# Kernel tuning notes

Measured on AMD Instinct MI355X. Metric: run time of the kernel, lower is better.

The kernel has to match this reference:

```python
import jax, jax.numpy as jnp
import numpy as np

N = 100000
E = 1600000
IN_FEATS = 256
OUT_FEATS = 128
THRESHOLD = 0.5


def setup_inputs() -> dict:
    key = jax.random.key(0)
    k1, k2, k3, k4, k5, k6, k7 = jax.random.split(key, 7)
    return {
        "feat": jax.random.normal(k1, (N, IN_FEATS), dtype=jnp.float32),
        "src": jax.random.randint(k2, (E,), 0, N, dtype=jnp.int32),
        "dst": jax.random.randint(k3, (E,), 0, N, dtype=jnp.int32),
        "edge_weight": jax.random.uniform(k4, (E,), dtype=jnp.float32),
        "weight": jax.random.normal(k5, (IN_FEATS, OUT_FEATS), dtype=jnp.float32),
        "bias": jax.random.normal(k6, (OUT_FEATS,), dtype=jnp.float32),
        "mask_real": jax.random.uniform(k7, (IN_FEATS, OUT_FEATS), dtype=jnp.float32),
    }


def reference(feat, src, dst, edge_weight, weight, bias, mask_real):
    ones_e = jnp.ones((E,), dtype=feat.dtype)
    # norm == 'both': scale source feats by out_degree^-0.5 (clamped at 1)
    out_deg = jnp.clip(jax.ops.segment_sum(ones_e, src, num_segments=N), 1.0)
    feat_src = feat * (out_deg ** -0.5)[:, None]  # [N, IN]
    # binarized mask with straight-through estimator (training-mode path)
    hard = (mask_real > THRESHOLD).astype(mask_real.dtype)
    mask_t = jax.lax.stop_gradient(hard - mask_real) + mask_real
    w = mask_t * weight  # [IN, OUT]
    # in_feats > out_feats: project before aggregation
    feat_src = feat_src @ w  # [N, OUT]
    # u_mul_e then sum: gather source feats, scale by edge weight, scatter-add to dst
    msgs = feat_src[src] * edge_weight[:, None]  # [E, OUT]
    rst = jax.ops.segment_sum(msgs, dst, num_segments=N)  # [N, OUT]
    # norm == 'both': scale by in_degree^-0.5 (clamped at 1)
    in_deg = jnp.clip(jax.ops.segment_sum(ones_e, dst, num_segments=N), 1.0)
    rst = rst * (in_deg ** -0.5)[:, None]
    return rst + bias
```

## Files before the change

### kernel.cpp

```cpp
#include <hip/hip_runtime.h>

#define N_NODES 100000
#define N_EDGES 1600000
#define IN_F 256
#define OUT_F 128
#define NBUCK 391
#define NPART 256
#define CHUNK (N_EDGES / NPART)
#define BCAP 5632

#define ODW2 12500
#define ODRB2 ((ODW2 + 255) / 256)

typedef __attribute__((ext_vector_type(8))) short short8;
typedef __attribute__((ext_vector_type(4))) float f32x4;

__device__ __forceinline__ unsigned bf16_rne(float f) {
    unsigned u = __float_as_uint(f);
    return (u + 0x7fffu + ((u >> 16) & 1u)) >> 16;
}

__global__ __launch_bounds__(1024) void fused_pre_kernel(const int* __restrict__ src,
                                                         const int* __restrict__ dst,
                                                         const float* __restrict__ weight,
                                                         const float* __restrict__ mask_real,
                                                         unsigned* __restrict__ part,
                                                         unsigned* __restrict__ hist,
                                                         unsigned short* __restrict__ wmT) {
    __shared__ unsigned h[ODW2];
    __shared__ unsigned hh[NBUCK];
    int b = blockIdx.x, t = threadIdx.x;
    for (int i = t; i < ODW2; i += 1024) h[i] = 0u;
    for (int i = t; i < NBUCK; i += 1024) hh[i] = 0u;
    if (t < 128) {
        int i = b * 128 + t;
        int k = i >> 7, n = i & 127;
        float v = (mask_real[i] > 0.5f) ? weight[i] : 0.0f;
        wmT[(size_t)n * IN_F + k] = (unsigned short)bf16_rne(v);
    }
    __syncthreads();
    int base = b * CHUNK;
    for (int i = t; i < CHUNK; i += 1024) {
        unsigned s = (unsigned)src[base + i];
        unsigned d = (unsigned)dst[base + i];
        atomicAdd(&h[s >> 3], 1u << ((s & 7u) * 4u));
        atomicAdd(&hh[d >> 8], 1u);
    }
    __syncthreads();
    unsigned* op = part + (size_t)b * ODW2;
    for (int i = t; i < ODW2; i += 1024) op[i] = h[i];
    for (int i = t; i < NBUCK; i += 1024) hist[(size_t)b * NBUCK + i] = hh[i];
}

__global__ __launch_bounds__(256) void fused_reduce_kernel(const unsigned* __restrict__ part,
                                                           const unsigned* __restrict__ hist,
                                                           unsigned* __restrict__ outpk,
                                                           unsigned* __restrict__ bsum,
                                                           unsigned* __restrict__ colscan) {
    __shared__ unsigned pscan[256];
    int t = threadIdx.x;
    if (blockIdx.x < ODRB2) {
        int d = blockIdx.x * 256 + t;
        if (d < ODW2) {
            unsigned sumE = 0u, sumO = 0u;
#pragma unroll 8
            for (int p = 0; p < NPART; p++) {
                unsigned v = part[(size_t)p * ODW2 + d];
                sumE += v & 0x0F0F0F0Fu;
                sumO += (v >> 4) & 0x0F0F0F0Fu;
            }
            unsigned w0 = (sumE & 0xFFu) | ((sumO & 0xFFu) << 8) |
                          ((sumE & 0xFF00u) << 8) | ((sumO & 0xFF00u) << 16);
            unsigned w1 = ((sumE >> 16) & 0xFFu) | (((sumO >> 16) & 0xFFu) << 8) |
                          (((sumE >> 24) & 0xFFu) << 16) | ((sumO >> 24) << 24);
            ((uint2*)outpk)[d] = make_uint2(w0, w1);
        }
    } else {
        int b = blockIdx.x - ODRB2;
        unsigned v = hist[(size_t)t * NBUCK + b];
        pscan[t] = v;
        __syncthreads();
#pragma unroll
        for (int d = 1; d < 256; d <<= 1) {
            unsigned x = (t >= d) ? pscan[t - d] : 0u;
            __syncthreads();
            pscan[t] += x;
            __syncthreads();
        }
        colscan[(size_t)b * 256 + t] = pscan[t] - v;
        if (t == 255) bsum[b] = pscan[255];
    }
}

__global__ __launch_bounds__(1024) void scatter_kernel(const int* __restrict__ src,
                                                       const int* __restrict__ dst,
                                                       const float* __restrict__ ew,
                                                       const unsigned* __restrict__ colscan,
                                                       const unsigned* __restrict__ bsum,
                                                       uint2* __restrict__ tmp) {
    __shared__ unsigned sc[1024];
    __shared__ unsigned cur[NBUCK];
    int p = blockIdx.x, t = threadIdx.x;
    unsigned v = (t < NBUCK) ? bsum[t] : 0u;
    sc[t] = v;
    __syncthreads();
#pragma unroll
    for (int d = 1; d < 1024; d <<= 1) {
        unsigned x = (t >= d) ? sc[t - d] : 0u;
        __syncthreads();
        sc[t] += x;
        __syncthreads();
    }
    if (t < NBUCK) cur[t] = (sc[t] - v) + colscan[(size_t)t * 256 + p];
    __syncthreads();
    int base = p * CHUNK;
    for (int i = t; i < CHUNK; i += 1024) {
        int e = base + i;
        int s = src[e];
        int d = dst[e];
        unsigned pos = atomicAdd(&cur[(unsigned)d >> 8], 1u);
        tmp[pos] = make_uint2((unsigned)s | (((unsigned)d & 255u) << 17),
                              __float_as_uint(ew[e]));
    }
}

__global__ __launch_bounds__(512) void gemm_kernel(const float* __restrict__ feat,
                                                   const unsigned short* __restrict__ wmT,
                                                   const unsigned char* __restrict__ outdeg8,
                                                   unsigned short* __restrict__ hb) {
    __shared__ unsigned short sB[128][264];
    int t = threadIdx.x;
    for (int idx = t; idx < (128 * 256 / 8); idx += 512) {
        int flat = idx * 8;
        *(uint4*)&sB[flat >> 8][flat & 255] = *(const uint4*)&wmT[flat];
    }
    __syncthreads();

    int lane = t & 63, wv = t >> 6;
    int m16 = lane & 15, quad = lane >> 4;
    int row0 = blockIdx.x * 128;
    int arow = min(row0 + wv * 16 + m16, N_NODES - 1);
    const float* fp = feat + (size_t)arow * IN_F + quad * 8;

    float4 va[16];
#pragma unroll
    for (int i = 0; i < 8; i++) {
        va[2 * i]     = *(const float4*)(fp + i * 32);
        va[2 * i + 1] = *(const float4*)(fp + i * 32 + 4);
    }

    f32x4 acc[8];
#pragma unroll
    for (int i = 0; i < 8; i++) acc[i] = (f32x4){0.f, 0.f, 0.f, 0.f};

#pragma unroll
    for (int i = 0; i < 8; i++) {
        uint4 pk;
        pk.x = bf16_rne(va[2 * i].x) | (bf16_rne(va[2 * i].y) << 16);
        pk.y = bf16_rne(va[2 * i].z) | (bf16_rne(va[2 * i].w) << 16);
        pk.z = bf16_rne(va[2 * i + 1].x) | (bf16_rne(va[2 * i + 1].y) << 16);
        pk.w = bf16_rne(va[2 * i + 1].z) | (bf16_rne(va[2 * i + 1].w) << 16);
        short8 a;
        *(uint4*)&a = pk;
#pragma unroll
        for (int nt = 0; nt < 8; nt++) {
            short8 b = *(const short8*)&sB[nt * 16 + m16][i * 32 + quad * 8];
            acc[nt] = __builtin_amdgcn_mfma_f32_16x16x32_bf16(a, b, acc[nt], 0, 0, 0);
        }
    }
#pragma unroll
    for (int reg = 0; reg < 4; reg++) {
        int row = row0 + wv * 16 + quad * 4 + reg;
        if (row < N_NODES) {
            float s = rsqrtf(fmaxf((float)outdeg8[row], 1.0f));
#pragma unroll
            for (int nt = 0; nt < 8; nt++)
                hb[(size_t)row * OUT_F + nt * 16 + m16] =
                    (unsigned short)bf16_rne(acc[nt][reg] * s);
        }
    }
}

__global__ __launch_bounds__(1024) void bucket_gather_kernel(const uint2* __restrict__ tmp,
                                                             const unsigned* __restrict__ bsum,
                                                             const uint4* __restrict__ hrows4,
                                                             const float* __restrict__ bias,
                                                             float* __restrict__ out) {
    __shared__ uint2 ebuf[BCAP];
    __shared__ unsigned sm[BCAP];
    __shared__ unsigned nstart[257];
    __shared__ unsigned hcnt[256];
    __shared__ unsigned red[1024];
    int b = blockIdx.x, t = threadIdx.x;

    unsigned loc = 0u;
    for (int i = t; i < b; i += 1024) loc += bsum[i];
    red[t] = loc;
    __syncthreads();
#pragma unroll
    for (int d = 512; d > 0; d >>= 1) {
        if (t < d) red[t] += red[t + d];
        __syncthreads();
    }
    unsigned base = red[0];
    unsigned next = base + bsum[b];
    int cnt = (int)(next - base);
    if (cnt > BCAP) cnt = BCAP;
    if (t < 256) hcnt[t] = 0u;
    for (int i = t; i < cnt; i += 1024) ebuf[i] = tmp[base + i];
    __syncthreads();
    for (int i = t; i < cnt; i += 1024) atomicAdd(&hcnt[ebuf[i].x >> 17], 1u);
    __syncthreads();
    unsigned v = (t < 256) ? hcnt[t] : 0u;
    if (t < 256) red[t] = v;
    __syncthreads();
#pragma unroll
    for (int d = 1; d < 256; d <<= 1) {
        unsigned x = (t < 256 && t >= d) ? red[t - d] : 0u;
        __syncthreads();
        if (t < 256) red[t] += x;
        __syncthreads();
    }
    if (t < 256) {
        unsigned excl = red[t] - v;
        nstart[t] = excl;
        hcnt[t] = excl;
    }
    if (t == 0) nstart[256] = (unsigned)cnt;
    __syncthreads();
    for (int i = t; i < cnt; i += 1024) {
        uint2 m = ebuf[i];
        unsigned pos = atomicAdd(&hcnt[m.x >> 17], 1u);
        sm[pos] = ((m.y + 0x10000u) & 0xFFFE0000u) | (m.x & 0x1FFFFu);
    }
    __syncthreads();

    int lane = t & 63, wv = t >> 6;
    int g = lane >> 4, q = lane & 15;
    for (int nn = wv * 16; nn < wv * 16 + 16; nn++) {
        int node = b * 256 + nn;
        if (node >= N_NODES) continue;
        unsigned beg = nstart[nn];
        int deg = (int)(nstart[nn + 1] - beg);

        float acc[8];
#pragma unroll
        for (int i = 0; i < 8; i++) acc[i] = 0.0f;

        for (int bs = 0; bs < deg; bs += 64) {
            int c = min(64, deg - bs);
            unsigned pv = (lane < c) ? sm[beg + bs + lane] : 0u;
            int nch = (c + 3) >> 2;
#pragma unroll 4
            for (int j = 0; j < nch; j++) {
                int ei = (j << 2) + g;
                unsigned p = __shfl(pv, ei);
                unsigned s = p & 0x1FFFFu;
                float w = __uint_as_float(p & 0xFFFE0000u);
                uint4 h = hrows4[(size_t)s * 16u + q];
                acc[0] = fmaf(__uint_as_float(h.x << 16), w, acc[0]);
                acc[1] = fmaf(__uint_as_float(h.x & 0xffff0000u), w, acc[1]);
                acc[2] = fmaf(__uint_as_float(h.y << 16), w, acc[2]);
                acc[3] = fmaf(__uint_as_float(h.y & 0xffff0000u), w, acc[3]);
                acc[4] = fmaf(__uint_as_float(h.z << 16), w, acc[4]);
                acc[5] = fmaf(__uint_as_float(h.z & 0xffff0000u), w, acc[5]);
                acc[6] = fmaf(__uint_as_float(h.w << 16), w, acc[6]);
                acc[7] = fmaf(__uint_as_float(h.w & 0xffff0000u), w, acc[7]);
            }
        }

#pragma unroll
        for (int i = 0; i < 8; i++) {
            acc[i] += __shfl_xor(acc[i], 16);
            acc[i] += __shfl_xor(acc[i], 32);
        }

        float o0, o1;
        if (g == 0)      { o0 = acc[0]; o1 = acc[1]; }
        else if (g == 1) { o0 = acc[2]; o1 = acc[3]; }
        else if (g == 2) { o0 = acc[4]; o1 = acc[5]; }
        else             { o0 = acc[6]; o1 = acc[7]; }

        float scale = rsqrtf(fmaxf((float)deg, 1.0f));
        int col = q * 8 + g * 2;
        float2 bb = *(const float2*)&bias[col];
        float2 o = make_float2(o0 * scale + bb.x, o1 * scale + bb.y);
        *(float2*)&out[(size_t)node * OUT_F + col] = o;
    }
}

extern "C" void kernel_launch(void* const* d_in, const int* in_sizes, int n_in,
                              void* d_out, int out_size, void* d_ws, size_t ws_size,
                              hipStream_t stream) {
    const float* feat      = (const float*)d_in[0];
    const int*   src       = (const int*)d_in[1];
    const int*   dst       = (const int*)d_in[2];
    const float* ew        = (const float*)d_in[3];
    const float* weight    = (const float*)d_in[4];
    const float* bias      = (const float*)d_in[5];
    const float* mask_real = (const float*)d_in[6];
    float* out = (float*)d_out;

    char* ws = (char*)d_ws;
    size_t o = 0;
    auto take = [&](size_t bytes) {
        char* p = ws + o;
        o = (o + bytes + 255) & ~(size_t)255;
        return p;
    };
    unsigned short* wmT     = (unsigned short*)take((size_t)IN_F * OUT_F * 2);
    unsigned*       outpk   = (unsigned*)take((size_t)25600 * 4);
    unsigned*       hist    = (unsigned*)take((size_t)NPART * NBUCK * 4);
    unsigned*       colscan = (unsigned*)take((size_t)NBUCK * 256 * 4);
    unsigned*       bsum    = (unsigned*)take((size_t)NBUCK * 4);
    uint2*          tmp     = (uint2*)take((size_t)N_EDGES * 8);
    unsigned short* hrows   = (unsigned short*)take((size_t)N_NODES * OUT_F * 2);

    unsigned* odpart = (unsigned*)tmp;

    fused_pre_kernel<<<NPART, 1024, 0, stream>>>(src, dst, weight, mask_real,
                                                 odpart, hist, wmT);
    fused_reduce_kernel<<<ODRB2 + NBUCK, 256, 0, stream>>>(odpart, hist, outpk,
                                                           bsum, colscan);
    scatter_kernel<<<NPART, 1024, 0, stream>>>(src, dst, ew, colscan, bsum, tmp);
    gemm_kernel<<<(N_NODES + 127) / 128, 512, 0, stream>>>(feat, wmT,
                                                           (const unsigned char*)outpk, hrows);
    bucket_gather_kernel<<<NBUCK, 1024, 0, stream>>>(tmp, bsum,
                                                     (const uint4*)hrows, bias, out);
}
```

Baseline: 300.6 us.

## Fuse degree, scan and scatter phases into one cooperative kernel; drop GEMM LDS staging

The pre-histogram, reduce/scan and edge scatter kernels are merged into a single cooperative kernel that uses grid-wide syncs between phases. This removes two kernel launches and the idle gaps between them. Separately, the GEMM no longer stages the masked weight matrix in LDS. It reads B fragments straight from global/L2 memory with smaller 256-thread blocks, and a sched_barrier keeps the feature loads grouped. The costs are the grid-sync overhead, a need for all 256 large blocks to be co-resident, and more global-memory traffic for B in the GEMM.

```diff
diff --git a/kernel.cpp b/kernel.cpp
--- a/kernel.cpp
+++ b/kernel.cpp
@@ -1,4 +1,7 @@
 #include <hip/hip_runtime.h>
+#include <hip/hip_cooperative_groups.h>
+
+namespace cg = cooperative_groups;
 
 #define N_NODES 100000
 #define N_EDGES 1600000
@@ -10,7 +13,6 @@
 #define BCAP 5632
 
 #define ODW2 12500
-#define ODRB2 ((ODW2 + 255) / 256)
 
 typedef __attribute__((ext_vector_type(8))) short short8;
 typedef __attribute__((ext_vector_type(4))) float f32x4;
@@ -20,16 +22,24 @@
     return (u + 0x7fffu + ((u >> 16) & 1u)) >> 16;
 }
 
-__global__ __launch_bounds__(1024) void fused_pre_kernel(const int* __restrict__ src,
-                                                         const int* __restrict__ dst,
-                                                         const float* __restrict__ weight,
-                                                         const float* __restrict__ mask_real,
-                                                         unsigned* __restrict__ part,
-                                                         unsigned* __restrict__ hist,
-                                                         unsigned short* __restrict__ wmT) {
+__global__ __launch_bounds__(1024) void prep_kernel(const int* __restrict__ src,
+                                                    const int* __restrict__ dst,
+                                                    const float* __restrict__ ew,
+                                                    const float* __restrict__ weight,
+                                                    const float* __restrict__ mask_real,
+                                                    unsigned* __restrict__ odpart,
+                                                    unsigned* __restrict__ hist,
+                                                    unsigned short* __restrict__ wmT,
+                                                    unsigned* __restrict__ outpk,
+                                                    unsigned* __restrict__ bsum,
+                                                    unsigned* __restrict__ colscan,
+                                                    uint2* __restrict__ tmp) {
+    cg::grid_group grid = cg::this_grid();
     __shared__ unsigned h[ODW2];
     __shared__ unsigned hh[NBUCK];
+    __shared__ unsigned sc[1024];
     int b = blockIdx.x, t = threadIdx.x;
+
     for (int i = t; i < ODW2; i += 1024) h[i] = 0u;
     for (int i = t; i < NBUCK; i += 1024) hh[i] = 0u;
     if (t < 128) {
@@ -47,25 +57,21 @@
         atomicAdd(&hh[d >> 8], 1u);
     }
     __syncthreads();
-    unsigned* op = part + (size_t)b * ODW2;
-    for (int i = t; i < ODW2; i += 1024) op[i] = h[i];
-    for (int i = t; i < NBUCK; i += 1024) hist[(size_t)b * NBUCK + i] = hh[i];
-}
-
-__global__ __launch_bounds__(256) void fused_reduce_kernel(const unsigned* __restrict__ part,
-                                                           const unsigned* __restrict__ hist,
-                                                           unsigned* __restrict__ outpk,
-                                                           unsigned* __restrict__ bsum,
-                                                           unsigned* __restrict__ colscan) {
-    __shared__ unsigned pscan[256];
-    int t = threadIdx.x;
-    if (blockIdx.x < ODRB2) {
-        int d = blockIdx.x * 256 + t;
-        if (d < ODW2) {
+    {
+        unsigned* op = odpart + (size_t)b * ODW2;
+        for (int i = t; i < ODW2; i += 1024) op[i] = h[i];
+        for (int i = t; i < NBUCK; i += 1024) hist[(size_t)b * NBUCK + i] = hh[i];
+    }
+
+    grid.sync();
+
+    if (b < 25) {
+        int d = b * 512 + t;
+        if (t < 512 && d < ODW2) {
             unsigned sumE = 0u, sumO = 0u;
 #pragma unroll 8
             for (int p = 0; p < NPART; p++) {
-                unsigned v = part[(size_t)p * ODW2 + d];
+                unsigned v = odpart[(size_t)p * ODW2 + d];
                 sumE += v & 0x0F0F0F0Fu;
                 sumO += (v >> 4) & 0x0F0F0F0Fu;
             }
@@ -76,71 +82,60 @@
             ((uint2*)outpk)[d] = make_uint2(w0, w1);
         }
     } else {
-        int b = blockIdx.x - ODRB2;
-        unsigned v = hist[(size_t)t * NBUCK + b];
-        pscan[t] = v;
-        __syncthreads();
-#pragma unroll
-        for (int d = 1; d < 256; d <<= 1) {
-            unsigned x = (t >= d) ? pscan[t - d] : 0u;
+        for (int c = b - 25; c < NBUCK; c += 231) {
+            unsigned v = (t < 256) ? hist[(size_t)t * NBUCK + c] : 0u;
+            if (t < 256) sc[t] = v;
             __syncthreads();
-            pscan[t] += x;
+#pragma unroll
+            for (int d = 1; d < 256; d <<= 1) {
+                unsigned x = (t < 256 && t >= d) ? sc[t - d] : 0u;
+                __syncthreads();
+                if (t < 256) sc[t] += x;
+                __syncthreads();
+            }
+            if (t < 256) colscan[(size_t)c * 256 + t] = sc[t] - v;
+            if (t == 255) bsum[c] = sc[255];
             __syncthreads();
         }
-        colscan[(size_t)b * 256 + t] = pscan[t] - v;
-        if (t == 255) bsum[b] = pscan[255];
-    }
-}
-
-__global__ __launch_bounds__(1024) void scatter_kernel(const int* __restrict__ src,
-                                                       const int* __restrict__ dst,
-                                                       const float* __restrict__ ew,
-                                                       const unsigned* __restrict__ colscan,
-                                                       const unsigned* __restrict__ bsum,
-                                                       uint2* __restrict__ tmp) {
-    __shared__ unsigned sc[1024];
-    __shared__ unsigned cur[NBUCK];
-    int p = blockIdx.x, t = threadIdx.x;
-    unsigned v = (t < NBUCK) ? bsum[t] : 0u;
-    sc[t] = v;
-    __syncthreads();
-#pragma unroll
-    for (int d = 1; d < 1024; d <<= 1) {
-        unsigned x = (t >= d) ? sc[t - d] : 0u;
-        __syncthreads();
-        sc[t] += x;
-        __syncthreads();
-    }
-    if (t < NBUCK) cur[t] = (sc[t] - v) + colscan[(size_t)t * 256 + p];
-    __syncthreads();
-    int base = p * CHUNK;
-    for (int i = t; i < CHUNK; i += 1024) {
-        int e = base + i;
-        int s = src[e];
-        int d = dst[e];
-        unsigned pos = atomicAdd(&cur[(unsigned)d >> 8], 1u);
-        tmp[pos] = make_uint2((unsigned)s | (((unsigned)d & 255u) << 17),
-                              __float_as_uint(ew[e]));
-    }
-}
-
-__global__ __launch_bounds__(512) void gemm_kernel(const float* __restrict__ feat,
+    }
+
+    grid.sync();
+
+    {
+        unsigned v = (t < NBUCK) ? bsum[t] : 0u;
+        sc[t] = v;
+        __syncthreads();
+#pragma unroll
+        for (int d = 1; d < 1024; d <<= 1) {
+            unsigned x = (t >= d) ? sc[t - d] : 0u;
+            __syncthreads();
+            sc[t] += x;
+            __syncthreads();
+        }
+        if (t < NBUCK) hh[t] = (sc[t] - v) + colscan[(size_t)t * 256 + b];
+        __syncthreads();
+        for (int i = t; i < CHUNK; i += 1024) {
+            int e = base + i;
+            int s = src[e];
+            int d = dst[e];
+            unsigned pos = atomicAdd(&hh[(unsigned)d >> 8], 1u);
+            tmp[pos] = make_uint2((unsigned)s | (((unsigned)d & 255u) << 17),
+                                  __float_as_uint(ew[e]));
+        }
+    }
+}
+
+__global__ __launch_bounds__(256) void gemm_kernel(const float* __restrict__ feat,
                                                    const unsigned short* __restrict__ wmT,
                                                    const unsigned char* __restrict__ outdeg8,
                                                    unsigned short* __restrict__ hb) {
-    __shared__ unsigned short sB[128][264];
     int t = threadIdx.x;
-    for (int idx = t; idx < (128 * 256 / 8); idx += 512) {
-        int flat = idx * 8;
-        *(uint4*)&sB[flat >> 8][flat & 255] = *(const uint4*)&wmT[flat];
-    }
-    __syncthreads();
-
     int lane = t & 63, wv = t >> 6;
     int m16 = lane & 15, quad = lane >> 4;
-    int row0 = blockIdx.x * 128;
+    int row0 = blockIdx.x * 64;
     int arow = min(row0 + wv * 16 + m16, N_NODES - 1);
     const float* fp = feat + (size_t)arow * IN_F + quad * 8;
+    const unsigned short* wb = wmT + (size_t)m16 * IN_F + quad * 8;
 
     float4 va[16];
 #pragma unroll
@@ -148,6 +143,7 @@
         va[2 * i]     = *(const float4*)(fp + i * 32);
         va[2 * i + 1] = *(const float4*)(fp + i * 32 + 4);
     }
+    __builtin_amdgcn_sched_barrier(0);
 
     f32x4 acc[8];
 #pragma unroll
@@ -164,8 +160,8 @@
         *(uint4*)&a = pk;
 #pragma unroll
         for (int nt = 0; nt < 8; nt++) {
-            short8 b = *(const short8*)&sB[nt * 16 + m16][i * 32 + quad * 8];
-            acc[nt] = __builtin_amdgcn_mfma_f32_16x16x32_bf16(a, b, acc[nt], 0, 0, 0);
+            short8 bfrag = *(const short8*)&wb[(size_t)(nt * 16) * IN_F + i * 32];
+            acc[nt] = __builtin_amdgcn_mfma_f32_16x16x32_bf16(a, bfrag, acc[nt], 0, 0, 0);
         }
     }
 #pragma unroll
@@ -318,13 +314,13 @@
 
     unsigned* odpart = (unsigned*)tmp;
 
-    fused_pre_kernel<<<NPART, 1024, 0, stream>>>(src, dst, weight, mask_real,
-                                                 odpart, hist, wmT);
-    fused_reduce_kernel<<<ODRB2 + NBUCK, 256, 0, stream>>>(odpart, hist, outpk,
-                                                           bsum, colscan);
-    scatter_kernel<<<NPART, 1024, 0, stream>>>(src, dst, ew, colscan, bsum, tmp);
-    gemm_kernel<<<(N_NODES + 127) / 128, 512, 0, stream>>>(feat, wmT,
-                                                           (const unsigned char*)outpk, hrows);
+    void* args[] = {(void*)&src, (void*)&dst, (void*)&ew, (void*)&weight,
+                    (void*)&mask_real, (void*)&odpart, (void*)&hist, (void*)&wmT,
+                    (void*)&outpk, (void*)&bsum, (void*)&colscan, (void*)&tmp};
+    hipLaunchCooperativeKernel((void*)prep_kernel, dim3(NPART), dim3(1024),
+                               args, 0, stream);
+    gemm_kernel<<<(N_NODES + 63) / 64, 256, 0, stream>>>(feat, wmT,
+                                                         (const unsigned char*)outpk, hrows);
     bucket_gather_kernel<<<NBUCK, 1024, 0, stream>>>(tmp, bsum,
                                                      (const uint4*)hrows, bias, out);
 }
```

New measurement: 417.1 us. +38.7%, slower.
